# Optimization experiments

Hardware: AMD Instinct MI355X
Metric: run time of the kernel (lower is better)

Reference implementation:

```python
import jax, jax.numpy as jnp
import numpy as np

B, N, C = 2, 2048, 1024
H = 16
D = C // H  # head_dim = 64
SCALE = D ** -0.5


def setup_inputs() -> dict:
    key = jax.random.key(0)
    k1, k2, k3, k4 = jax.random.split(key, 4)
    x = jax.random.normal(k1, (B, N, C), dtype=jnp.float32)
    # nn.Linear(in_dim, 3*out_dim, bias=False): store as [in, 3*out] for x @ W
    w_qkv = jax.random.normal(k2, (C, 3 * C), dtype=jnp.float32) * (C ** -0.5)
    w_proj = jax.random.normal(k3, (C, C), dtype=jnp.float32) * (C ** -0.5)
    b_proj = jax.random.normal(k4, (C,), dtype=jnp.float32) * 0.01
    return {"x": x, "w_qkv": w_qkv, "w_proj": w_proj, "b_proj": b_proj}


def reference(x, w_qkv, w_proj, b_proj):
    b, n, c = x.shape
    # QKV projection -> [3, B, H, N, D]
    qkv = (x @ w_qkv).reshape(b, n, 3, H, D).transpose(2, 0, 3, 1, 4)
    q, k, v = qkv[0], qkv[1], qkv[2]
    # scaled dot-product attention, full [B, H, N, N] scores as in original
    attn = jax.nn.softmax(jnp.einsum('bhqd,bhkd->bhqk', q * SCALE, k), axis=-1)
    out = jnp.einsum('bhqk,bhkd->bhqd', attn, v)  # [B, H, N, D]
    out = out.transpose(0, 2, 1, 3).reshape(b, n, c)
    return out @ w_proj + b_proj
```

## Files before the change

### kernel.cpp

```cpp
#include <hip/hip_runtime.h>

typedef unsigned short u16;
typedef float f32x4 __attribute__((ext_vector_type(4)));
typedef short bf16x8 __attribute__((ext_vector_type(8)));
typedef u16 u16x4 __attribute__((ext_vector_type(4)));
typedef u16 u16x8 __attribute__((ext_vector_type(8)));
typedef __bf16 bfr4 __attribute__((ext_vector_type(4)));

#define BB 2
#define NN 2048
#define CC 1024
#define HH 16
#define DD 64
#define MM (BB * NN)
#define NQKV (3 * CC)
#define QSCALE 0.18033688011112042f

#if __has_builtin(__builtin_amdgcn_exp2f)
#define EXP2(x) __builtin_amdgcn_exp2f(x)
#else
#define EXP2(x) exp2f(x)
#endif

__device__ __forceinline__ u16 f2bf(float f) {
    unsigned u = __float_as_uint(f);
    u += 0x7FFFu + ((u >> 16) & 1u);
    return (u16)(u >> 16);
}

__device__ __forceinline__ void ld_lds16(const u16* g, u16* l) {
    __builtin_amdgcn_global_load_lds(
        (const __attribute__((address_space(1))) unsigned int*)g,
        (__attribute__((address_space(3))) unsigned int*)l, 16, 0, 0);
}

__global__ __launch_bounds__(256) void k_tobf(const float* __restrict__ in,
                                              u16* __restrict__ out, int n) {
    int i = (blockIdx.x * 256 + threadIdx.x) * 8;
    if (i >= n) return;
    float4 a = *(const float4*)(in + i);
    float4 b = *(const float4*)(in + i + 4);
    u16x8 o;
    o[0] = f2bf(a.x); o[1] = f2bf(a.y); o[2] = f2bf(a.z); o[3] = f2bf(a.w);
    o[4] = f2bf(b.x); o[5] = f2bf(b.y); o[6] = f2bf(b.z); o[7] = f2bf(b.w);
    *(u16x8*)(out + i) = o;
}

__global__ __launch_bounds__(256) void k_tcast(const float* __restrict__ in,
                                               u16* __restrict__ out,
                                               int K, int Nn) {
    __shared__ float tile[32][33];
    int t = threadIdx.x, tx = t & 31, ty = t >> 5;
    int n0 = blockIdx.x * 32, k0 = blockIdx.y * 32;
#pragma unroll
    for (int r = 0; r < 32; r += 8)
        tile[ty + r][tx] = in[(size_t)(k0 + ty + r) * Nn + n0 + tx];
    __syncthreads();
#pragma unroll
    for (int r = 0; r < 32; r += 8)
        out[(size_t)(n0 + ty + r) * K + k0 + tx] = f2bf(tile[tx][ty + r]);
}

template <int MODE>
__global__ __launch_bounds__(256) void k_gemm(
    const u16* __restrict__ A, const u16* __restrict__ B,
    u16* __restrict__ Qb, u16* __restrict__ Kb, u16* __restrict__ Vb,
    const float* __restrict__ bias, float* __restrict__ Cout) {
    const int Kd = 1024;
    __shared__ __align__(16) u16 Ah[128][32];
    __shared__ __align__(16) u16 Bh[128][32];

    int t = threadIdx.x;
    int wave = t >> 6, lane = t & 63;
    int quad = lane >> 4, l16 = lane & 15;
    int wm = (wave >> 1) * 64, wn = (wave & 1) * 64;
    int m0 = blockIdx.y * 128, n0 = blockIdx.x * 128;

    int strow0 = wave * 16 + (lane >> 2);
    int stdst  = (lane & 3) * 8;
    int stsrc  = ((lane & 3) ^ ((lane >> 3) & 3)) * 8;
    int cfrag = (quad ^ ((l16 >> 1) & 3)) * 8;

    f32x4 acc[4][4];
#pragma unroll
    for (int i = 0; i < 4; i++)
#pragma unroll
        for (int j = 0; j < 4; j++) acc[i][j] = f32x4{0.f, 0.f, 0.f, 0.f};

    for (int k0 = 0; k0 < Kd; k0 += 32) {
        __syncthreads();
#pragma unroll
        for (int ii = 0; ii < 2; ii++) {
            int row = strow0 + ii * 64;
            ld_lds16(A + (size_t)(m0 + row) * Kd + k0 + stsrc, &Ah[row][stdst]);
            ld_lds16(B + (size_t)(n0 + row) * Kd + k0 + stsrc, &Bh[row][stdst]);
        }
        __syncthreads();

        bf16x8 af[4], bf[4];
#pragma unroll
        for (int i = 0; i < 4; i++) {
            af[i] = *(const bf16x8*)&Ah[wm + i * 16 + l16][cfrag];
            bf[i] = *(const bf16x8*)&Bh[wn + i * 16 + l16][cfrag];
        }
#pragma unroll
        for (int mi = 0; mi < 4; mi++)
#pragma unroll
            for (int ni = 0; ni < 4; ni++)
                acc[mi][ni] = __builtin_amdgcn_mfma_f32_16x16x32_bf16(
                    af[mi], bf[ni], acc[mi][ni], 0, 0, 0);
    }

#pragma unroll
    for (int mi = 0; mi < 4; mi++)
#pragma unroll
        for (int ni = 0; ni < 4; ni++)
#pragma unroll
            for (int r = 0; r < 4; r++) {
                int grow = m0 + wm + mi * 16 + quad * 4 + r;
                int gcol = n0 + wn + ni * 16 + l16;
                float v = acc[mi][ni][r];
                if (MODE == 0) {
                    int three = gcol >> 10, rem = gcol & 1023;
                    int h = rem >> 6, d = rem & 63;
                    int bb = grow >> 11, nn = grow & 2047;
                    if (three == 0) {
                        Qb[((size_t)(bb * HH + h) * NN + nn) * DD + d] = f2bf(v * QSCALE);
                    } else if (three == 1) {
                        Kb[((size_t)(bb * HH + h) * NN + nn) * DD + d] = f2bf(v);
                    } else {
                        Vb[((size_t)(bb * HH + h) * DD + d) * NN + nn] = f2bf(v);
                    }
                } else {
                    Cout[(size_t)grow * CC + gcol] = v + bias[gcol];
                }
            }
}

__global__ __launch_bounds__(256) void k_attn(const u16* __restrict__ Qb,
                                              const u16* __restrict__ Kb,
                                              const u16* __restrict__ VbT,
                                              u16* __restrict__ Ob) {
    __shared__ __align__(16) u16 Ks[64][64];
    __shared__ __align__(16) u16 Vs[64][64];
    __shared__ __align__(16) u16 Ps[4][32][72];

    int t = threadIdx.x, wave = t >> 6, lane = t & 63;
    int quad = lane >> 4, l16 = lane & 15;
    int bh = blockIdx.y, q0 = blockIdx.x * 128;
    const size_t kbase = (size_t)bh * NN * DD;
    const size_t vbase = (size_t)bh * DD * NN;

    bf16x8 qf[2][2];
#pragma unroll
    for (int qj = 0; qj < 2; qj++) {
        int qrow = q0 + wave * 32 + qj * 16 + l16;
        qf[qj][0] = *(const bf16x8*)&Qb[kbase + (size_t)qrow * DD + quad * 8];
        qf[qj][1] = *(const bf16x8*)&Qb[kbase + (size_t)qrow * DD + 32 + quad * 8];
    }

    f32x4 o[4][2];
#pragma unroll
    for (int i = 0; i < 4; i++)
#pragma unroll
        for (int j = 0; j < 2; j++) o[i][j] = f32x4{0.f, 0.f, 0.f, 0.f};
    float lrow[2] = {0.f, 0.f};

    int stgrp = lane & 7;
    int stsrc = (stgrp ^ (lane >> 3)) * 8;
    int strow0 = wave * 8 + (lane >> 3);
    int cf0 = (quad ^ (l16 & 7)) * 8;
    int cf1 = ((4 + quad) ^ (l16 & 7)) * 8;

    for (int c = 0; c < NN / 64; c++) {
        __syncthreads();
#pragma unroll
        for (int ii = 0; ii < 2; ii++) {
            int row = strow0 + ii * 32;
            ld_lds16(&Kb[kbase + (size_t)(c * 64 + row) * DD + stsrc], &Ks[row][stgrp * 8]);
            ld_lds16(&VbT[vbase + (size_t)row * NN + c * 64 + stsrc], &Vs[row][stgrp * 8]);
        }
        __syncthreads();

        bf16x8 kf[4][2];
#pragma unroll
        for (int kt = 0; kt < 4; kt++) {
            kf[kt][0] = *(const bf16x8*)&Ks[kt * 16 + l16][cf0];
            kf[kt][1] = *(const bf16x8*)&Ks[kt * 16 + l16][cf1];
        }

#pragma unroll
        for (int qj = 0; qj < 2; qj++) {
            f32x4 s[4];
#pragma unroll
            for (int kt = 0; kt < 4; kt++) {
                f32x4 z = f32x4{0.f, 0.f, 0.f, 0.f};
                z = __builtin_amdgcn_mfma_f32_16x16x32_bf16(kf[kt][0], qf[qj][0], z, 0, 0, 0);
                z = __builtin_amdgcn_mfma_f32_16x16x32_bf16(kf[kt][1], qf[qj][1], z, 0, 0, 0);
                s[kt] = z;
            }
            float sum = lrow[qj];
#pragma unroll
            for (int kt = 0; kt < 4; kt++) {
                bfr4 pk;
#pragma unroll
                for (int r = 0; r < 4; r++) {
                    float e = EXP2(s[kt][r]);
                    sum += e;
                    pk[r] = (__bf16)e;
                }
                *(bfr4*)&Ps[wave][qj * 16 + l16][kt * 16 + quad * 4] = pk;
            }
            lrow[qj] = sum;
        }
        __asm__ volatile("s_waitcnt lgkmcnt(0)" ::: "memory");
        bf16x8 pb[2][2];
#pragma unroll
        for (int qj = 0; qj < 2; qj++) {
            pb[qj][0] = *(const bf16x8*)&Ps[wave][qj * 16 + l16][quad * 8];
            pb[qj][1] = *(const bf16x8*)&Ps[wave][qj * 16 + l16][32 + quad * 8];
        }
#pragma unroll
        for (int dt = 0; dt < 4; dt++) {
            bf16x8 vf0 = *(const bf16x8*)&Vs[dt * 16 + l16][cf0];
            bf16x8 vf1 = *(const bf16x8*)&Vs[dt * 16 + l16][cf1];
#pragma unroll
            for (int qj = 0; qj < 2; qj++) {
                o[dt][qj] = __builtin_amdgcn_mfma_f32_16x16x32_bf16(vf0, pb[qj][0], o[dt][qj], 0, 0, 0);
                o[dt][qj] = __builtin_amdgcn_mfma_f32_16x16x32_bf16(vf1, pb[qj][1], o[dt][qj], 0, 0, 0);
            }
        }
    }

    int b = bh >> 4, h = bh & 15;
#pragma unroll
    for (int qj = 0; qj < 2; qj++) {
        float l = lrow[qj];
        l += __shfl_xor(l, 16, 64);
        l += __shfl_xor(l, 32, 64);
        float inv = 1.f / l;
        int grow = b * NN + q0 + wave * 32 + qj * 16 + l16;
#pragma unroll
        for (int dt = 0; dt < 4; dt++) {
            u16x4 hv;
#pragma unroll
            for (int r = 0; r < 4; r++) hv[r] = f2bf(o[dt][qj][r] * inv);
            int gcol = h * DD + dt * 16 + quad * 4;
            *(u16x4*)&Ob[(size_t)grow * CC + gcol] = hv;
        }
    }
}

extern "C" void kernel_launch(void* const* d_in, const int* in_sizes, int n_in,
                              void* d_out, int out_size, void* d_ws, size_t ws_size,
                              hipStream_t stream) {
    const float* x      = (const float*)d_in[0];
    const float* w_qkv  = (const float*)d_in[1];
    const float* w_proj = (const float*)d_in[2];
    const float* b_proj = (const float*)d_in[3];
    float* out = (float*)d_out;

    u16* p = (u16*)d_ws;
    u16* Xb = p; p += (size_t)MM * CC;
    u16* Wq = p; p += (size_t)NQKV * CC;
    u16* Wp = p; p += (size_t)CC * CC;
    u16* Qb = p; p += (size_t)MM * CC;
    u16* Kb = p; p += (size_t)MM * CC;
    u16* Vb = p; p += (size_t)MM * CC;
    u16* Ob = p; p += (size_t)MM * CC;

    k_tobf<<<(MM * CC) / (256 * 8), 256, 0, stream>>>(x, Xb, MM * CC);
    k_tcast<<<dim3(NQKV / 32, CC / 32), 256, 0, stream>>>(w_qkv, Wq, CC, NQKV);
    k_tcast<<<dim3(CC / 32, CC / 32), 256, 0, stream>>>(w_proj, Wp, CC, CC);
    k_gemm<0><<<dim3(NQKV / 128, MM / 128), 256, 0, stream>>>(
        Xb, Wq, Qb, Kb, Vb, nullptr, nullptr);
    k_attn<<<dim3(NN / 128, BB * HH), 256, 0, stream>>>(Qb, Kb, Vb, Ob);
    k_gemm<1><<<dim3(CC / 128, MM / 128), 256, 0, stream>>>(
        Ob, Wp, nullptr, nullptr, nullptr, b_proj, out);
}
```

Baseline: 199.7 us.

## Double-buffer K/V tiles in attention and raise wave priority around MFMA blocks

The attention kernel now keeps two LDS buffers for the K and V tiles. It issues the async global-to-LDS load for the next tile before computing on the current one, which drops one of the two barriers per iteration and hides load latency behind the QK^T, softmax and PV work. It also wraps the MFMA sections in s_setprio so waves doing matrix math get scheduling priority. The cost is 16KB more LDS per block, which could lower occupancy.

```diff
diff --git a/kernel.cpp b/kernel.cpp
--- a/kernel.cpp
+++ b/kernel.cpp
@@ -141,8 +141,8 @@
                                               const u16* __restrict__ Kb,
                                               const u16* __restrict__ VbT,
                                               u16* __restrict__ Ob) {
-    __shared__ __align__(16) u16 Ks[64][64];
-    __shared__ __align__(16) u16 Vs[64][64];
+    __shared__ __align__(16) u16 Ks[2][64][64];
+    __shared__ __align__(16) u16 Vs[2][64][64];
     __shared__ __align__(16) u16 Ps[4][32][72];
 
     int t = threadIdx.x, wave = t >> 6, lane = t & 63;
@@ -172,26 +172,36 @@
     int cf0 = (quad ^ (l16 & 7)) * 8;
     int cf1 = ((4 + quad) ^ (l16 & 7)) * 8;
 
+#define STAGE(cc, bb_)                                                         \
+    {                                                                          \
+        _Pragma("unroll")                                                      \
+        for (int ii = 0; ii < 2; ii++) {                                       \
+            int row = strow0 + ii * 32;                                        \
+            ld_lds16(&Kb[kbase + (size_t)((cc) * 64 + row) * DD + stsrc],      \
+                     &Ks[bb_][row][stgrp * 8]);                                \
+            ld_lds16(&VbT[vbase + (size_t)row * NN + (cc) * 64 + stsrc],       \
+                     &Vs[bb_][row][stgrp * 8]);                                \
+        }                                                                      \
+    }
+
+    STAGE(0, 0);
+    __syncthreads();
+
+    int cur = 0;
     for (int c = 0; c < NN / 64; c++) {
-        __syncthreads();
-#pragma unroll
-        for (int ii = 0; ii < 2; ii++) {
-            int row = strow0 + ii * 32;
-            ld_lds16(&Kb[kbase + (size_t)(c * 64 + row) * DD + stsrc], &Ks[row][stgrp * 8]);
-            ld_lds16(&VbT[vbase + (size_t)row * NN + c * 64 + stsrc], &Vs[row][stgrp * 8]);
-        }
-        __syncthreads();
+        if (c + 1 < NN / 64) STAGE(c + 1, cur ^ 1);
 
         bf16x8 kf[4][2];
 #pragma unroll
         for (int kt = 0; kt < 4; kt++) {
-            kf[kt][0] = *(const bf16x8*)&Ks[kt * 16 + l16][cf0];
-            kf[kt][1] = *(const bf16x8*)&Ks[kt * 16 + l16][cf1];
+            kf[kt][0] = *(const bf16x8*)&Ks[cur][kt * 16 + l16][cf0];
+            kf[kt][1] = *(const bf16x8*)&Ks[cur][kt * 16 + l16][cf1];
         }
 
 #pragma unroll
         for (int qj = 0; qj < 2; qj++) {
             f32x4 s[4];
+            __builtin_amdgcn_s_setprio(1);
 #pragma unroll
             for (int kt = 0; kt < 4; kt++) {
                 f32x4 z = f32x4{0.f, 0.f, 0.f, 0.f};
@@ -199,6 +209,7 @@
                 z = __builtin_amdgcn_mfma_f32_16x16x32_bf16(kf[kt][1], qf[qj][1], z, 0, 0, 0);
                 s[kt] = z;
             }
+            __builtin_amdgcn_s_setprio(0);
             float sum = lrow[qj];
 #pragma unroll
             for (int kt = 0; kt < 4; kt++) {
@@ -220,17 +231,23 @@
             pb[qj][0] = *(const bf16x8*)&Ps[wave][qj * 16 + l16][quad * 8];
             pb[qj][1] = *(const bf16x8*)&Ps[wave][qj * 16 + l16][32 + quad * 8];
         }
+        __builtin_amdgcn_s_setprio(1);
 #pragma unroll
         for (int dt = 0; dt < 4; dt++) {
-            bf16x8 vf0 = *(const bf16x8*)&Vs[dt * 16 + l16][cf0];
-            bf16x8 vf1 = *(const bf16x8*)&Vs[dt * 16 + l16][cf1];
+            bf16x8 vf0 = *(const bf16x8*)&Vs[cur][dt * 16 + l16][cf0];
+            bf16x8 vf1 = *(const bf16x8*)&Vs[cur][dt * 16 + l16][cf1];
 #pragma unroll
             for (int qj = 0; qj < 2; qj++) {
                 o[dt][qj] = __builtin_amdgcn_mfma_f32_16x16x32_bf16(vf0, pb[qj][0], o[dt][qj], 0, 0, 0);
                 o[dt][qj] = __builtin_amdgcn_mfma_f32_16x16x32_bf16(vf1, pb[qj][1], o[dt][qj], 0, 0, 0);
             }
         }
-    }
+        __builtin_amdgcn_s_setprio(0);
+
+        __syncthreads();
+        cur ^= 1;
+    }
+#undef STAGE
 
     int b = bh >> 4, h = bh & 15;
 #pragma unroll
```

Result: no change. 202.3 us (+1.3%).

## Double-buffer K/V tiles and use eight waves per attention block

Applied to the files above, without the earlier changes.

The attention kernel now runs with 512 threads, where each of eight waves owns 16 query rows instead of 32. K and V tiles are ping-ponged across two LDS buffers so the load of the next chunk overlaps compute on the current one, and one barrier per chunk is dropped. s_setprio is raised around the MFMA sections. The trade is less register reuse of K/V fragments per wave and more LDS, in exchange for more waves to hide latency. Softmax still skips max subtraction, as before.

```diff
diff --git a/kernel.cpp b/kernel.cpp
--- a/kernel.cpp
+++ b/kernel.cpp
@@ -137,13 +137,13 @@
             }
 }
 
-__global__ __launch_bounds__(256) void k_attn(const u16* __restrict__ Qb,
+__global__ __launch_bounds__(512) void k_attn(const u16* __restrict__ Qb,
                                               const u16* __restrict__ Kb,
                                               const u16* __restrict__ VbT,
                                               u16* __restrict__ Ob) {
-    __shared__ __align__(16) u16 Ks[64][64];
-    __shared__ __align__(16) u16 Vs[64][64];
-    __shared__ __align__(16) u16 Ps[4][32][72];
+    __shared__ __align__(16) u16 Ks0[64][64], Ks1[64][64];
+    __shared__ __align__(16) u16 Vs0[64][64], Vs1[64][64];
+    __shared__ __align__(16) u16 Ps[8][16][72];
 
     int t = threadIdx.x, wave = t >> 6, lane = t & 63;
     int quad = lane >> 4, l16 = lane & 15;
@@ -151,103 +151,95 @@
     const size_t kbase = (size_t)bh * NN * DD;
     const size_t vbase = (size_t)bh * DD * NN;
 
-    bf16x8 qf[2][2];
-#pragma unroll
-    for (int qj = 0; qj < 2; qj++) {
-        int qrow = q0 + wave * 32 + qj * 16 + l16;
-        qf[qj][0] = *(const bf16x8*)&Qb[kbase + (size_t)qrow * DD + quad * 8];
-        qf[qj][1] = *(const bf16x8*)&Qb[kbase + (size_t)qrow * DD + 32 + quad * 8];
-    }
-
-    f32x4 o[4][2];
-#pragma unroll
-    for (int i = 0; i < 4; i++)
-#pragma unroll
-        for (int j = 0; j < 2; j++) o[i][j] = f32x4{0.f, 0.f, 0.f, 0.f};
-    float lrow[2] = {0.f, 0.f};
+    int qrow = q0 + wave * 16 + l16;
+    bf16x8 qf0 = *(const bf16x8*)&Qb[kbase + (size_t)qrow * DD + quad * 8];
+    bf16x8 qf1 = *(const bf16x8*)&Qb[kbase + (size_t)qrow * DD + 32 + quad * 8];
+
+    f32x4 o[4];
+#pragma unroll
+    for (int i = 0; i < 4; i++) o[i] = f32x4{0.f, 0.f, 0.f, 0.f};
+    f32x4 lrow = f32x4{0.f, 0.f, 0.f, 0.f};
 
     int stgrp = lane & 7;
     int stsrc = (stgrp ^ (lane >> 3)) * 8;
-    int strow0 = wave * 8 + (lane >> 3);
+    int strow = wave * 8 + (lane >> 3);
     int cf0 = (quad ^ (l16 & 7)) * 8;
     int cf1 = ((4 + quad) ^ (l16 & 7)) * 8;
 
-    for (int c = 0; c < NN / 64; c++) {
-        __syncthreads();
-#pragma unroll
-        for (int ii = 0; ii < 2; ii++) {
-            int row = strow0 + ii * 32;
-            ld_lds16(&Kb[kbase + (size_t)(c * 64 + row) * DD + stsrc], &Ks[row][stgrp * 8]);
-            ld_lds16(&VbT[vbase + (size_t)row * NN + c * 64 + stsrc], &Vs[row][stgrp * 8]);
-        }
-        __syncthreads();
-
+    auto STAGE = [&](int cc, u16 (*Kd_)[64], u16 (*Vd_)[64]) {
+        ld_lds16(&Kb[kbase + (size_t)(cc * 64 + strow) * DD + stsrc],
+                 &Kd_[strow][stgrp * 8]);
+        ld_lds16(&VbT[vbase + (size_t)strow * NN + cc * 64 + stsrc],
+                 &Vd_[strow][stgrp * 8]);
+    };
+
+    auto COMPUTE = [&](u16 (*Ksrc)[64], u16 (*Vsrc)[64]) {
         bf16x8 kf[4][2];
 #pragma unroll
         for (int kt = 0; kt < 4; kt++) {
-            kf[kt][0] = *(const bf16x8*)&Ks[kt * 16 + l16][cf0];
-            kf[kt][1] = *(const bf16x8*)&Ks[kt * 16 + l16][cf1];
-        }
-
-#pragma unroll
-        for (int qj = 0; qj < 2; qj++) {
-            f32x4 s[4];
-#pragma unroll
-            for (int kt = 0; kt < 4; kt++) {
-                f32x4 z = f32x4{0.f, 0.f, 0.f, 0.f};
-                z = __builtin_amdgcn_mfma_f32_16x16x32_bf16(kf[kt][0], qf[qj][0], z, 0, 0, 0);
-                z = __builtin_amdgcn_mfma_f32_16x16x32_bf16(kf[kt][1], qf[qj][1], z, 0, 0, 0);
-                s[kt] = z;
+            kf[kt][0] = *(const bf16x8*)&Ksrc[kt * 16 + l16][cf0];
+            kf[kt][1] = *(const bf16x8*)&Ksrc[kt * 16 + l16][cf1];
+        }
+        f32x4 s[4];
+        __builtin_amdgcn_s_setprio(1);
+#pragma unroll
+        for (int kt = 0; kt < 4; kt++) {
+            f32x4 z = f32x4{0.f, 0.f, 0.f, 0.f};
+            z = __builtin_amdgcn_mfma_f32_16x16x32_bf16(kf[kt][0], qf0, z, 0, 0, 0);
+            z = __builtin_amdgcn_mfma_f32_16x16x32_bf16(kf[kt][1], qf1, z, 0, 0, 0);
+            s[kt] = z;
+        }
+        __builtin_amdgcn_s_setprio(0);
+#pragma unroll
+        for (int kt = 0; kt < 4; kt++) {
+            bfr4 pk;
+#pragma unroll
+            for (int r = 0; r < 4; r++) {
+                float e = EXP2(s[kt][r]);
+                lrow[r] += e;
+                pk[r] = (__bf16)e;
             }
-            float sum = lrow[qj];
-#pragma unroll
-            for (int kt = 0; kt < 4; kt++) {
-                bfr4 pk;
-#pragma unroll
-                for (int r = 0; r < 4; r++) {
-                    float e = EXP2(s[kt][r]);
-                    sum += e;
-                    pk[r] = (__bf16)e;
-                }
-                *(bfr4*)&Ps[wave][qj * 16 + l16][kt * 16 + quad * 4] = pk;
-            }
-            lrow[qj] = sum;
+            *(bfr4*)&Ps[wave][l16][kt * 16 + quad * 4] = pk;
         }
         __asm__ volatile("s_waitcnt lgkmcnt(0)" ::: "memory");
-        bf16x8 pb[2][2];
-#pragma unroll
-        for (int qj = 0; qj < 2; qj++) {
-            pb[qj][0] = *(const bf16x8*)&Ps[wave][qj * 16 + l16][quad * 8];
-            pb[qj][1] = *(const bf16x8*)&Ps[wave][qj * 16 + l16][32 + quad * 8];
-        }
+        bf16x8 pb0 = *(const bf16x8*)&Ps[wave][l16][quad * 8];
+        bf16x8 pb1 = *(const bf16x8*)&Ps[wave][l16][32 + quad * 8];
+        __builtin_amdgcn_s_setprio(1);
 #pragma unroll
         for (int dt = 0; dt < 4; dt++) {
-            bf16x8 vf0 = *(const bf16x8*)&Vs[dt * 16 + l16][cf0];
-            bf16x8 vf1 = *(const bf16x8*)&Vs[dt * 16 + l16][cf1];
-#pragma unroll
-            for (int qj = 0; qj < 2; qj++) {
-                o[dt][qj] = __builtin_amdgcn_mfma_f32_16x16x32_bf16(vf0, pb[qj][0], o[dt][qj], 0, 0, 0);
-                o[dt][qj] = __builtin_amdgcn_mfma_f32_16x16x32_bf16(vf1, pb[qj][1], o[dt][qj], 0, 0, 0);
-            }
-        }
+            bf16x8 vf0 = *(const bf16x8*)&Vsrc[dt * 16 + l16][cf0];
+            bf16x8 vf1 = *(const bf16x8*)&Vsrc[dt * 16 + l16][cf1];
+            o[dt] = __builtin_amdgcn_mfma_f32_16x16x32_bf16(vf0, pb0, o[dt], 0, 0, 0);
+            o[dt] = __builtin_amdgcn_mfma_f32_16x16x32_bf16(vf1, pb1, o[dt], 0, 0, 0);
+        }
+        __builtin_amdgcn_s_setprio(0);
+    };
+
+    STAGE(0, Ks0, Vs0);
+    __syncthreads();
+
+    for (int c = 0; c < NN / 64; c += 2) {
+        STAGE(c + 1, Ks1, Vs1);
+        COMPUTE(Ks0, Vs0);
+        __syncthreads();
+        if (c + 2 < NN / 64) STAGE(c + 2, Ks0, Vs0);
+        COMPUTE(Ks1, Vs1);
+        __syncthreads();
     }
 
     int b = bh >> 4, h = bh & 15;
-#pragma unroll
-    for (int qj = 0; qj < 2; qj++) {
-        float l = lrow[qj];
-        l += __shfl_xor(l, 16, 64);
-        l += __shfl_xor(l, 32, 64);
-        float inv = 1.f / l;
-        int grow = b * NN + q0 + wave * 32 + qj * 16 + l16;
-#pragma unroll
-        for (int dt = 0; dt < 4; dt++) {
-            u16x4 hv;
-#pragma unroll
-            for (int r = 0; r < 4; r++) hv[r] = f2bf(o[dt][qj][r] * inv);
-            int gcol = h * DD + dt * 16 + quad * 4;
-            *(u16x4*)&Ob[(size_t)grow * CC + gcol] = hv;
-        }
+    float l = (lrow[0] + lrow[1]) + (lrow[2] + lrow[3]);
+    l += __shfl_xor(l, 16, 64);
+    l += __shfl_xor(l, 32, 64);
+    float inv = 1.f / l;
+    int grow = b * NN + q0 + wave * 16 + l16;
+#pragma unroll
+    for (int dt = 0; dt < 4; dt++) {
+        u16x4 hv;
+#pragma unroll
+        for (int r = 0; r < 4; r++) hv[r] = f2bf(o[dt][r] * inv);
+        int gcol = h * DD + dt * 16 + quad * 4;
+        *(u16x4*)&Ob[(size_t)grow * CC + gcol] = hv;
     }
 }
 
@@ -274,7 +266,7 @@
     k_tcast<<<dim3(CC / 32, CC / 32), 256, 0, stream>>>(w_proj, Wp, CC, CC);
     k_gemm<0><<<dim3(NQKV / 128, MM / 128), 256, 0, stream>>>(
         Xb, Wq, Qb, Kb, Vb, nullptr, nullptr);
-    k_attn<<<dim3(NN / 128, BB * HH), 256, 0, stream>>>(Qb, Kb, Vb, Ob);
+    k_attn<<<dim3(NN / 128, BB * HH), 512, 0, stream>>>(Qb, Kb, Vb, Ob);
     k_gemm<1><<<dim3(CC / 128, MM / 128), 256, 0, stream>>>(
         Ob, Wp, nullptr, nullptr, nullptr, b_proj, out);
 }
```

Result: faster. 191.4 us (-4.1%).
